# Kernel tuning notes

Measured on AMD Instinct MI355X. Metric: run time of the kernel, lower is better.

Reference implementation:

```python
import jax, jax.numpy as jnp
import numpy as np

N_NODES = 50000
N_EDGES = 300000
HEADS = 2
OUT_CH = 128
BN_EPS = 1e-5
NEG_SLOPE = 0.2


def _batchnorm(x, g, b):
    # training-mode BatchNorm1d: biased batch statistics
    mean = x.mean(axis=0)
    var = x.var(axis=0)
    return (x - mean) * jax.lax.rsqrt(var + BN_EPS) * g + b


def _gatv2(x, src, dst, edge_attr, Wl, bl, Wr, br, We, att, bias, concat):
    # PyG GATv2Conv, share_weights=False, aggr='add'
    n = x.shape[0]
    xl = (x @ Wl + bl).reshape(n, HEADS, OUT_CH)  # source messages
    xr = (x @ Wr + br).reshape(n, HEADS, OUT_CH)  # destination term
    ee = (edge_attr @ We).reshape(-1, HEADS, OUT_CH)
    s = jax.nn.leaky_relu(xl[src] + xr[dst] + ee, NEG_SLOPE)  # [E,H,C]
    alpha = jnp.einsum('ehc,hc->eh', s, att)  # [E,H]
    # segment softmax over edges grouped by destination node
    m = jax.ops.segment_max(alpha, dst, num_segments=n)
    a = jnp.exp(alpha - m[dst])
    den = jax.ops.segment_sum(a, dst, num_segments=n)
    a = a / (den[dst] + 1e-16)
    out = jax.ops.segment_sum(xl[src] * a[:, :, None], dst, num_segments=n)  # [N,H,C]
    out = out.reshape(n, HEADS * OUT_CH) if concat else out.mean(axis=1)
    return out + bias


def setup_inputs() -> dict:
    key = jax.random.key(0)
    ks = jax.random.split(key, 16)
    d = {}
    d['h'] = jax.random.normal(ks[0], (N_NODES, 5), jnp.float32)
    d['edge_index'] = jax.random.randint(ks[1], (2, N_EDGES), 0, N_NODES, jnp.int64)
    d['edge_weight'] = jax.random.uniform(ks[2], (N_EDGES, 1), jnp.float32)
    d['bn0_g'] = jnp.ones((5,), jnp.float32)
    d['bn0_b'] = jnp.zeros((5,), jnp.float32)
    d['bn1_g'] = jnp.ones((256,), jnp.float32)
    d['bn1_b'] = jnp.zeros((256,), jnp.float32)
    def lin(k, fan_in, fan_out):
        return jax.random.normal(k, (fan_in, fan_out), jnp.float32) * (1.0 / np.sqrt(fan_in))
    # conv1: in=5 -> heads*out=256, concat=True
    d['c1_Wl'] = lin(ks[3], 5, 256); d['c1_bl'] = jnp.zeros((256,), jnp.float32)
    d['c1_Wr'] = lin(ks[4], 5, 256); d['c1_br'] = jnp.zeros((256,), jnp.float32)
    d['c1_We'] = lin(ks[5], 1, 256)
    d['c1_att'] = jax.random.normal(ks[6], (HEADS, OUT_CH), jnp.float32) * 0.1
    d['c1_bias'] = jnp.zeros((256,), jnp.float32)
    # mu: in=256 -> 128, concat=False
    d['mu_Wl'] = lin(ks[7], 256, 256); d['mu_bl'] = jnp.zeros((256,), jnp.float32)
    d['mu_Wr'] = lin(ks[8], 256, 256); d['mu_br'] = jnp.zeros((256,), jnp.float32)
    d['mu_We'] = lin(ks[9], 1, 256)
    d['mu_att'] = jax.random.normal(ks[10], (HEADS, OUT_CH), jnp.float32) * 0.1
    d['mu_bias'] = jnp.zeros((128,), jnp.float32)
    # log_std: same shapes as mu
    d['ls_Wl'] = lin(ks[11], 256, 256); d['ls_bl'] = jnp.zeros((256,), jnp.float32)
    d['ls_Wr'] = lin(ks[12], 256, 256); d['ls_br'] = jnp.zeros((256,), jnp.float32)
    d['ls_We'] = lin(ks[13], 1, 256)
    d['ls_att'] = jax.random.normal(ks[14], (HEADS, OUT_CH), jnp.float32) * 0.1
    d['ls_bias'] = jnp.zeros((128,), jnp.float32)
    return d


def reference(h, edge_index, edge_weight, bn0_g, bn0_b, bn1_g, bn1_b,
              c1_Wl, c1_bl, c1_Wr, c1_br, c1_We, c1_att, c1_bias,
              mu_Wl, mu_bl, mu_Wr, mu_br, mu_We, mu_att, mu_bias,
              ls_Wl, ls_bl, ls_Wr, ls_br, ls_We, ls_att, ls_bias):
    src, dst = edge_index[0], edge_index[1]
    x = _batchnorm(h, bn0_g, bn0_b)
    x = _gatv2(x, src, dst, edge_weight, c1_Wl, c1_bl, c1_Wr, c1_br, c1_We, c1_att, c1_bias, concat=True)
    x = jax.nn.relu(_batchnorm(x, bn1_g, bn1_b))
    # dropout identity (eval / deterministic)
    mu = _gatv2(x, src, dst, edge_weight, mu_Wl, mu_bl, mu_Wr, mu_br, mu_We, mu_att, mu_bias, concat=False)
    log_std = _gatv2(x, src, dst, edge_weight, ls_Wl, ls_bl, ls_Wr, ls_br, ls_We, ls_att, ls_bias, concat=False)
    return (mu, log_std)
```

## Files before the change

kernel.cpp:

```cpp
#include <hip/hip_runtime.h>
#include <math.h>

#define N_NODES 50000
#define N_EDGES 300000
#define BN_EPS 1e-5f
#define NEG_SLOPE 0.2f

#define RB_COUNT 3128
#define SCAN_TILES 49
#define BN1_BLOCKS 523

typedef short bf8v __attribute__((ext_vector_type(8)));
typedef float f4v __attribute__((ext_vector_type(4)));
typedef unsigned short u8v __attribute__((ext_vector_type(8)));

__device__ inline unsigned short f2bf(float f) {
    union { float f; unsigned u; } c; c.f = f;
    unsigned r = c.u + 0x7fffu + ((c.u >> 16) & 1u);
    return (unsigned short)(r >> 16);
}
__device__ inline float bf2f(unsigned short u) {
    union { unsigned u; float f; } c; c.u = ((unsigned)u) << 16;
    return c.f;
}

__device__ inline void async_copy16(void* lds, const void* g) {
    __builtin_amdgcn_global_load_lds(
        (const __attribute__((address_space(1))) unsigned int*)g,
        (__attribute__((address_space(3))) unsigned int*)lds, 16, 0, 0);
}

__global__ void bn0_reduce(const float* __restrict__ h, float* __restrict__ acc ) {
    __shared__ float lds[4][10];
    int tid = threadIdx.x;
    int lane = tid & 63, wave = tid >> 6;
    float ls[5] = {0,0,0,0,0}, lq[5] = {0,0,0,0,0};
    for (int r = blockIdx.x * 256 + tid; r < N_NODES; r += 128 * 256) {
        #pragma unroll
        for (int k = 0; k < 5; k++) {
            float v = h[r*5 + k];
            ls[k] += v; lq[k] += v*v;
        }
    }
    #pragma unroll
    for (int k = 0; k < 5; k++) {
        #pragma unroll
        for (int m = 1; m <= 32; m <<= 1) {
            ls[k] += __shfl_xor(ls[k], m, 64);
            lq[k] += __shfl_xor(lq[k], m, 64);
        }
    }
    if (lane == 0) {
        #pragma unroll
        for (int k = 0; k < 5; k++) { lds[wave][k] = ls[k]; lds[wave][5+k] = lq[k]; }
    }
    __syncthreads();
    if (tid < 10) {
        float s = lds[0][tid] + lds[1][tid] + lds[2][tid] + lds[3][tid];
        atomicAdd(&acc[tid], s);
    }
}

__global__ void bn0_finalize(const float* __restrict__ acc, const float* __restrict__ g,
                             const float* __restrict__ b, float* __restrict__ ss) {
    int tid = threadIdx.x;
    if (tid < 5) {
        float mean = acc[tid] * (1.f / N_NODES);
        float var  = acc[5 + tid] * (1.f / N_NODES) - mean*mean;
        float sc = g[tid] * rsqrtf(var + BN_EPS);
        ss[tid]     = sc;
        ss[5 + tid] = b[tid] - mean * sc;
    }
}

__global__ void bn0_apply(const float* __restrict__ h, const float* __restrict__ ss,
                          float* __restrict__ x0) {
    int i = blockIdx.x * blockDim.x + threadIdx.x;
    if (i < N_NODES * 5) {
        int k = i % 5;
        x0[i] = h[i] * ss[k] + ss[5 + k];
    }
}

__global__ void edge_count(const int* __restrict__ dst, int* __restrict__ count) {
    int e = blockIdx.x * blockDim.x + threadIdx.x;
    if (e < N_EDGES) atomicAdd(&count[dst[e]], 1);
}

__global__ void local_scan(const int* __restrict__ count, int* __restrict__ offsets,
                           int* __restrict__ tileSum) {
    __shared__ int lds[1024];
    int tid = threadIdx.x;
    int i = blockIdx.x * 1024 + tid;
    int v = (i < N_NODES) ? count[i] : 0;
    lds[tid] = v;
    __syncthreads();
    #pragma unroll
    for (int off = 1; off < 1024; off <<= 1) {
        int t = (tid >= off) ? lds[tid - off] : 0;
        __syncthreads();
        lds[tid] += t;
        __syncthreads();
    }
    if (i < N_NODES) offsets[i] = lds[tid] - v;
    if (tid == 1023) tileSum[blockIdx.x] = lds[1023];
}

__global__ void tile_scan(const int* __restrict__ tileSum, int* __restrict__ tilePrefix,
                          int* __restrict__ offsets) {
    int lane = threadIdx.x;
    int v = (lane < SCAN_TILES) ? tileSum[lane] : 0;
    int inc = v;
    #pragma unroll
    for (int off = 1; off < 64; off <<= 1) {
        int t = __shfl_up(inc, off, 64);
        if (lane >= off) inc += t;
    }
    int excl = inc - v;
    if (lane < SCAN_TILES) tilePrefix[lane] = excl;
    if (lane == SCAN_TILES - 1) offsets[N_NODES] = inc;
}

__global__ void add_prefix(int* __restrict__ offsets, const int* __restrict__ tilePrefix,
                           int* __restrict__ cursor) {
    int i = blockIdx.x * 1024 + threadIdx.x;
    if (i < N_NODES) {
        int o = offsets[i] + tilePrefix[blockIdx.x];
        offsets[i] = o;
        cursor[i] = o;
    }
}

__global__ void edge_scatter(const int* __restrict__ dst, const int* __restrict__ src,
                             const float* __restrict__ ew, int* __restrict__ cursor,
                             int* __restrict__ srcp, float* __restrict__ ewp) {
    int e = blockIdx.x * blockDim.x + threadIdx.x;
    if (e < N_EDGES) {
        int pos = atomicAdd(&cursor[dst[e]], 1);
        srcp[pos] = src[e];
        ewp[pos] = ew[e];
    }
}

__global__ void gemm_k5(const float* __restrict__ x0,
                        const float* __restrict__ Wl, const float* __restrict__ bl,
                        const float* __restrict__ Wr, const float* __restrict__ br,
                        unsigned short* __restrict__ xl, unsigned short* __restrict__ xr) {
    int n = blockIdx.x;
    int c = threadIdx.x;
    float a0 = x0[n*5+0], a1 = x0[n*5+1], a2 = x0[n*5+2], a3 = x0[n*5+3], a4 = x0[n*5+4];
    float l = bl[c] + a0*Wl[c] + a1*Wl[256+c] + a2*Wl[512+c] + a3*Wl[768+c] + a4*Wl[1024+c];
    float r = br[c] + a0*Wr[c] + a1*Wr[256+c] + a2*Wr[512+c] + a3*Wr[768+c] + a4*Wr[1024+c];
    xl[n*256 + c] = f2bf(l);
    xr[n*256 + c] = f2bf(r);
}

__global__ void pack_x_bn(const float* __restrict__ x, const float* __restrict__ ss1,
                          unsigned short* __restrict__ ap) {
    int t = blockIdx.x * 256 + threadIdx.x;
    int lane = t & 63;
    int kc = (t >> 6) & 7;
    int rb = t >> 9;
    int row = rb * 16 + (lane & 15);
    int k0 = kc * 32 + (lane >> 4) * 8;
    union { unsigned short h[8]; uint4 u; } tmp;
    if (row < N_NODES) {
        const float* s = x + (size_t)row * 256 + k0;
        #pragma unroll
        for (int j = 0; j < 8; j++) {
            int c = k0 + j;
            float v = s[j] * ss1[c] + ss1[256 + c];
            v = v > 0.f ? v : 0.f;
            tmp.h[j] = f2bf(v);
        }
    } else {
        #pragma unroll
        for (int j = 0; j < 8; j++) tmp.h[j] = 0;
    }
    *reinterpret_cast<uint4*>(ap + (size_t)t * 8) = tmp.u;
}

__global__ void pack_w(const float* __restrict__ Wl0, const float* __restrict__ Wr0,
                       const float* __restrict__ Wl1, const float* __restrict__ Wr1,
                       unsigned short* __restrict__ bp) {
    int t = blockIdx.x * 256 + threadIdx.x;
    int lane = t & 63;
    int nt = (t >> 6) & 31;
    int kc = (t >> 11) & 7;
    int conv = t >> 14;
    int col = nt * 16 + (lane & 15);
    int k0 = kc * 32 + (lane >> 4) * 8;
    const float* W = conv ? (col < 256 ? Wl1 : Wr1) : (col < 256 ? Wl0 : Wr0);
    int c = col & 255;
    union { unsigned short h[8]; uint4 u; } tmp;
    #pragma unroll
    for (int j = 0; j < 8; j++) tmp.h[j] = f2bf(W[(size_t)(k0 + j) * 256 + c]);
    *reinterpret_cast<uint4*>(bp + (size_t)t * 8) = tmp.u;
}

__global__ __launch_bounds__(512) void gemm_mfma(const unsigned short* __restrict__ ap,
        const unsigned short* __restrict__ bp,
        const float* __restrict__ bl, const float* __restrict__ br,
        unsigned short* __restrict__ xl, unsigned short* __restrict__ xr) {
    __shared__ unsigned short Bs[2][32][512];
    int lane = threadIdx.x & 63;
    int wave = threadIdx.x >> 6;
    int h = wave & 1;
    int rb = blockIdx.x * 4 + (wave >> 1);

    const unsigned short* aptr = ap + (size_t)rb * 4096 + lane * 8;
    const unsigned short* bsrc = bp + lane * 8;

    auto stage = [&](int buf, int kc) {
        #pragma unroll
        for (int j = 0; j < 4; j++) {
            int f = wave * 4 + j;
            async_copy16(&Bs[buf][f][lane * 8], bsrc + (size_t)kc * 16384 + f * 512);
        }
    };
    stage(0, 0);

    bf8v a[8];
    #pragma unroll
    for (int kc = 0; kc < 8; kc++) a[kc] = *reinterpret_cast<const bf8v*>(aptr + kc * 512);

    f4v acc[16];
    #pragma unroll
    for (int t = 0; t < 16; t++) acc[t] = (f4v){0.f, 0.f, 0.f, 0.f};

    for (int kc = 0; kc < 8; kc++) {
        __syncthreads();
        if (kc < 7) stage((kc + 1) & 1, kc + 1);
        const unsigned short* bb = &Bs[kc & 1][h * 16][lane * 8];
        #pragma unroll
        for (int t = 0; t < 16; t++) {
            bf8v b = *reinterpret_cast<const bf8v*>(bb + t * 512);
            acc[t] = __builtin_amdgcn_mfma_f32_16x16x32_bf16(a[kc], b, acc[t], 0, 0, 0);
        }
    }

    int c15 = lane & 15;
    int row0 = rb * 16 + (lane >> 4) * 4;
    unsigned short* outp = h ? xr : xl;
    const float* bias = h ? br : bl;
    #pragma unroll
    for (int t = 0; t < 16; t++) {
        int col = t * 16 + c15;
        float bv = bias[col];
        #pragma unroll
        for (int r = 0; r < 4; r++) {
            int row = row0 + r;
            if (row < N_NODES) outp[(size_t)row * 256 + col] = f2bf(acc[t][r] + bv);
        }
    }
}

template <int CONCAT>
__global__ void agg_fused(const unsigned short* __restrict__ xl,
                          const unsigned short* __restrict__ xr,
                          const float* __restrict__ We, const float* __restrict__ att,
                          const int* __restrict__ offsets, const int* __restrict__ srcp,
                          const float* __restrict__ ewp, const float* __restrict__ bias,
                          float* __restrict__ out) {
    int n = blockIdx.x * 4 + (threadIdx.x >> 6);
    int lane = threadIdx.x & 63;
    if (n >= N_NODES) return;
    int half = lane >> 5;
    int sub  = lane & 31;
    int cb   = (sub >> 4) * 128 + (sub & 15) * 8;
    float wv[8], av[8], rv[8];
    *(float4*)&wv[0] = *(const float4*)(We + cb);
    *(float4*)&wv[4] = *(const float4*)(We + cb + 4);
    *(float4*)&av[0] = *(const float4*)(att + cb);
    *(float4*)&av[4] = *(const float4*)(att + cb + 4);
    u8v r8 = *(const u8v*)(xr + (size_t)n * 256 + cb);
    #pragma unroll
    for (int j = 0; j < 8; j++) rv[j] = bf2f(r8[j]);
    int beg = offsets[n], end = offsets[n + 1];
    float mrun = -1e30f, den = 0.f;
    float acc[8];
    #pragma unroll
    for (int j = 0; j < 8; j++) acc[j] = 0.f;

    int i = beg + half;
    int sN = 0; float wN = 0.f;
    u8v lN;
    #pragma unroll
    for (int j = 0; j < 8; j++) lN[j] = 0;
    if (i < end) {
        sN = srcp[i]; wN = ewp[i];
        lN = *(const u8v*)(xl + (size_t)sN * 256 + cb);
    }
    for (; i < end; i += 2) {
        u8v l8 = lN; float w = wN;
        int nx = i + 2;
        if (nx < end) {
            sN = srcp[nx]; wN = ewp[nx];
            lN = *(const u8v*)(xl + (size_t)sN * 256 + cb);
        }
        float lv[8];
        float a = 0.f;
        #pragma unroll
        for (int j = 0; j < 8; j++) {
            lv[j] = bf2f(l8[j]);
            float v = lv[j] + rv[j] + w * wv[j];
            v = fmaxf(v, NEG_SLOPE * v);
            a += v * av[j];
        }
        a += __shfl_xor(a, 1, 64);
        a += __shfl_xor(a, 2, 64);
        a += __shfl_xor(a, 4, 64);
        a += __shfl_xor(a, 8, 64);
        float nm = fmaxf(mrun, a);
        float scl = __expf(mrun - nm);
        float p = __expf(a - nm);
        den = den * scl + p;
        #pragma unroll
        for (int j = 0; j < 8; j++) acc[j] = acc[j] * scl + p * lv[j];
        mrun = nm;
    }
    {
        float mo  = __shfl_xor(mrun, 32, 64);
        float dno = __shfl_xor(den, 32, 64);
        float nm = fmaxf(mrun, mo);
        float s0 = __expf(mrun - nm);
        float s1 = __expf(mo - nm);
        den = den * s0 + dno * s1;
        #pragma unroll
        for (int j = 0; j < 8; j++) {
            float ao = __shfl_xor(acc[j], 32, 64);
            acc[j] = acc[j] * s0 + ao * s1;
        }
    }
    float inv = 1.f / (den + 1e-16f);
    if (CONCAT) {
        if (lane < 32) {
            float o[8];
            #pragma unroll
            for (int j = 0; j < 8; j++) o[j] = acc[j] * inv + bias[cb + j];
            *(float4*)(out + (size_t)n * 256 + cb)     = *(float4*)&o[0];
            *(float4*)(out + (size_t)n * 256 + cb + 4) = *(float4*)&o[4];
        }
    } else {
        float o[8];
        #pragma unroll
        for (int j = 0; j < 8; j++) o[j] = acc[j] * inv;
        float po[8];
        #pragma unroll
        for (int j = 0; j < 8; j++) po[j] = __shfl_xor(o[j], 16, 64);
        if (lane < 16) {
            int c0 = (lane & 15) * 8;
            float r[8];
            #pragma unroll
            for (int j = 0; j < 8; j++) r[j] = (o[j] + po[j]) * 0.5f + bias[c0 + j];
            *(float4*)(out + (size_t)n * 128 + c0)     = *(float4*)&r[0];
            *(float4*)(out + (size_t)n * 128 + c0 + 4) = *(float4*)&r[4];
        }
    }
}

__global__ void bn1_reduce(const float* __restrict__ x, float* __restrict__ part) {
    __shared__ float lds[256][9];
    int tid = threadIdx.x;
    int cg = tid & 63;
    int ph = tid >> 6;
    int r0 = blockIdx.x * 96;
    float s[4] = {0,0,0,0}, q[4] = {0,0,0,0};
    #pragma unroll
    for (int it = 0; it < 24; it++) {
        int row = r0 + it * 4 + ph;
        if (row < N_NODES) {
            float4 v = *(const float4*)(x + (size_t)row * 256 + cg * 4);
            s[0] += v.x; s[1] += v.y; s[2] += v.z; s[3] += v.w;
            q[0] += v.x*v.x; q[1] += v.y*v.y; q[2] += v.z*v.z; q[3] += v.w*v.w;
        }
    }
    #pragma unroll
    for (int j = 0; j < 4; j++) { lds[tid][j] = s[j]; lds[tid][4+j] = q[j]; }
    __syncthreads();
    if (tid < 64) {
        float4 sv, qv;
        float* svp = (float*)&sv; float* qvp = (float*)&qv;
        #pragma unroll
        for (int j = 0; j < 4; j++) {
            svp[j] = lds[tid][j] + lds[tid+64][j] + lds[tid+128][j] + lds[tid+192][j];
            qvp[j] = lds[tid][4+j] + lds[tid+64][4+j] + lds[tid+128][4+j] + lds[tid+192][4+j];
        }
        *(float4*)(part + (size_t)blockIdx.x * 512 + cg * 4) = sv;
        *(float4*)(part + (size_t)blockIdx.x * 512 + 256 + cg * 4) = qv;
    }
}

__global__ void bn1_finalize(const float* __restrict__ part, const float* __restrict__ g,
                             const float* __restrict__ b, float* __restrict__ ss1) {
    __shared__ float lds[8][64];
    int t = threadIdx.x;
    int c = blockIdx.x * 32 + (t & 31);
    int ph = t >> 5;
    float s = 0.f, q = 0.f;
    for (int bi = ph; bi < BN1_BLOCKS; bi += 8) {
        s += part[(size_t)bi * 512 + c];
        q += part[(size_t)bi * 512 + 256 + c];
    }
    lds[ph][t & 31] = s;
    lds[ph][32 + (t & 31)] = q;
    __syncthreads();
    if (t < 32) {
        float ss = 0.f, qq = 0.f;
        #pragma unroll
        for (int p = 0; p < 8; p++) { ss += lds[p][t]; qq += lds[p][32 + t]; }
        float mean = ss * (1.f / N_NODES);
        float var  = qq * (1.f / N_NODES) - mean * mean;
        float sc = g[c] * rsqrtf(var + BN_EPS);
        ss1[c] = sc;
        ss1[256 + c] = b[c] - mean * sc;
    }
}

extern "C" void kernel_launch(void* const* d_in, const int* in_sizes, int n_in,
                              void* d_out, int out_size, void* d_ws, size_t ws_size,
                              hipStream_t stream) {
    const float* h          = (const float*)d_in[0];
    const int*   edge_index = (const int*)d_in[1];
    const int*   src = edge_index;
    const int*   dst = edge_index + N_EDGES;
    const float* ew   = (const float*)d_in[2];
    const float* bn0g = (const float*)d_in[3];
    const float* bn0b = (const float*)d_in[4];
    const float* bn1g = (const float*)d_in[5];
    const float* bn1b = (const float*)d_in[6];
    const float* c1_Wl = (const float*)d_in[7];
    const float* c1_bl = (const float*)d_in[8];
    const float* c1_Wr = (const float*)d_in[9];
    const float* c1_br = (const float*)d_in[10];
    const float* c1_We = (const float*)d_in[11];
    const float* c1_att = (const float*)d_in[12];
    const float* c1_bias = (const float*)d_in[13];
    const float* mu_Wl = (const float*)d_in[14];
    const float* mu_bl = (const float*)d_in[15];
    const float* mu_Wr = (const float*)d_in[16];
    const float* mu_br = (const float*)d_in[17];
    const float* mu_We = (const float*)d_in[18];
    const float* mu_att = (const float*)d_in[19];
    const float* mu_bias = (const float*)d_in[20];
    const float* ls_Wl = (const float*)d_in[21];
    const float* ls_bl = (const float*)d_in[22];
    const float* ls_Wr = (const float*)d_in[23];
    const float* ls_br = (const float*)d_in[24];
    const float* ls_We = (const float*)d_in[25];
    const float* ls_att = (const float*)d_in[26];
    const float* ls_bias = (const float*)d_in[27];

    float* out_mu = (float*)d_out;
    float* out_ls = (float*)d_out + (size_t)N_NODES * 128;

    char* ws = (char*)d_ws;
    size_t off = 0;
    auto alloc = [&](size_t bytes) -> void* {
        void* p = ws + off;
        off += (bytes + 255) / 256 * 256;
        return p;
    };
    float* x0      = (float*)alloc((size_t)N_NODES * 5 * 4);
    unsigned short* xl = (unsigned short*)alloc((size_t)N_NODES * 256 * 2);
    unsigned short* xr = (unsigned short*)alloc((size_t)N_NODES * 256 * 2);
    float* xB      = (float*)alloc((size_t)N_NODES * 256 * 4);
    float* bn0acc  = (float*)alloc(10 * 4);
    float* bn0ss   = (float*)alloc(10 * 4);
    float* bn1part = (float*)alloc((size_t)BN1_BLOCKS * 512 * 4);
    float* bn1ss   = (float*)alloc(512 * 4);
    int*   count   = (int*)alloc((size_t)N_NODES * 4);
    int*   offsets = (int*)alloc((size_t)(N_NODES + 1) * 4);
    int*   cursor  = (int*)alloc((size_t)N_NODES * 4);
    int*   srcp    = (int*)alloc((size_t)N_EDGES * 4);
    float* ewp     = (float*)alloc((size_t)N_EDGES * 4);
    int*   tileSum = (int*)alloc((size_t)SCAN_TILES * 4);
    int*   tilePre = (int*)alloc((size_t)SCAN_TILES * 4);
    unsigned short* Apack = (unsigned short*)alloc((size_t)RB_COUNT * 4096 * 2);
    unsigned short* Bpack = (unsigned short*)alloc((size_t)2 * 131072 * 2);

    hipMemsetAsync(count, 0, (size_t)N_NODES * 4, stream);
    hipMemsetAsync(bn0acc, 0, 10 * 4, stream);

    bn0_reduce<<<128, 256, 0, stream>>>(h, bn0acc);
    bn0_finalize<<<1, 64, 0, stream>>>(bn0acc, bn0g, bn0b, bn0ss);
    bn0_apply<<<(N_NODES * 5 + 255) / 256, 256, 0, stream>>>(h, bn0ss, x0);

    edge_count<<<(N_EDGES + 255) / 256, 256, 0, stream>>>(dst, count);
    local_scan<<<SCAN_TILES, 1024, 0, stream>>>(count, offsets, tileSum);
    tile_scan<<<1, 64, 0, stream>>>(tileSum, tilePre, offsets);
    add_prefix<<<SCAN_TILES, 1024, 0, stream>>>(offsets, tilePre, cursor);
    edge_scatter<<<(N_EDGES + 255) / 256, 256, 0, stream>>>(dst, src, ew, cursor, srcp, ewp);

    pack_w<<<128, 256, 0, stream>>>(mu_Wl, mu_Wr, ls_Wl, ls_Wr, Bpack);

    gemm_k5<<<N_NODES, 256, 0, stream>>>(x0, c1_Wl, c1_bl, c1_Wr, c1_br, xl, xr);
    agg_fused<1><<<N_NODES / 4 + 1, 256, 0, stream>>>(xl, xr, c1_We, c1_att, offsets,
                                                      srcp, ewp, c1_bias, xB);

    bn1_reduce<<<BN1_BLOCKS, 256, 0, stream>>>(xB, bn1part);
    bn1_finalize<<<8, 256, 0, stream>>>(bn1part, bn1g, bn1b, bn1ss);
    pack_x_bn<<<6256, 256, 0, stream>>>(xB, bn1ss, Apack);

    gemm_mfma<<<782, 512, 0, stream>>>(Apack, Bpack, mu_bl, mu_br, xl, xr);
    agg_fused<0><<<N_NODES / 4 + 1, 256, 0, stream>>>(xl, xr, mu_We, mu_att, offsets,
                                                      srcp, ewp, mu_bias, out_mu);

    gemm_mfma<<<782, 512, 0, stream>>>(Apack, Bpack + 131072, ls_bl, ls_br, xl, xr);
    agg_fused<0><<<N_NODES / 4 + 1, 256, 0, stream>>>(xl, xr, ls_We, ls_att, offsets,
                                                      srcp, ewp, ls_bias, out_ls);
}
```

Baseline: 453.5 us.

## Fuse mu/log_std aggregation into one dual kernel, fold BN0 into first GEMM

Both second-layer GEMMs now run before a single agg_dual kernel that walks each node's edge list once and aggregates the mu and log_std heads together. This shares the srcp/ewp loads and the loop overhead, and raises memory-level parallelism per gathered edge. The second GEMM writes into the xB buffer, which is reused because it is dead after pack_x_bn. BN0 apply is folded into gemm_k5, which now computes two packed bf16 outputs per thread. The aggregation math uses float2 vectors so packed FP32 instructions can be emitted. The dual kernel holds more live registers, which may lower occupancy.

```diff
diff --git a/kernel.cpp b/kernel.cpp
--- a/kernel.cpp
+++ b/kernel.cpp
@@ -12,16 +12,20 @@
 
 typedef short bf8v __attribute__((ext_vector_type(8)));
 typedef float f4v __attribute__((ext_vector_type(4)));
-typedef unsigned short u8v __attribute__((ext_vector_type(8)));
+typedef float f2v __attribute__((ext_vector_type(2)));
 
 __device__ inline unsigned short f2bf(float f) {
     union { float f; unsigned u; } c; c.f = f;
     unsigned r = c.u + 0x7fffu + ((c.u >> 16) & 1u);
     return (unsigned short)(r >> 16);
 }
-__device__ inline float bf2f(unsigned short u) {
-    union { unsigned u; float f; } c; c.u = ((unsigned)u) << 16;
-    return c.f;
+
+__device__ inline f2v bfpair(unsigned u) {
+    union { unsigned u; float f; } lo, hi;
+    lo.u = u << 16;
+    hi.u = u & 0xffff0000u;
+    f2v r; r.x = lo.f; r.y = hi.f;
+    return r;
 }
 
 __device__ inline void async_copy16(void* lds, const void* g) {
@@ -73,15 +77,6 @@
     }
 }
 
-__global__ void bn0_apply(const float* __restrict__ h, const float* __restrict__ ss,
-                          float* __restrict__ x0) {
-    int i = blockIdx.x * blockDim.x + threadIdx.x;
-    if (i < N_NODES * 5) {
-        int k = i % 5;
-        x0[i] = h[i] * ss[k] + ss[5 + k];
-    }
-}
-
 __global__ void edge_count(const int* __restrict__ dst, int* __restrict__ count) {
     int e = blockIdx.x * blockDim.x + threadIdx.x;
     if (e < N_EDGES) atomicAdd(&count[dst[e]], 1);
@@ -142,17 +137,27 @@
     }
 }
 
-__global__ void gemm_k5(const float* __restrict__ x0,
+__global__ void gemm_k5(const float* __restrict__ h, const float* __restrict__ ss,
                         const float* __restrict__ Wl, const float* __restrict__ bl,
                         const float* __restrict__ Wr, const float* __restrict__ br,
                         unsigned short* __restrict__ xl, unsigned short* __restrict__ xr) {
     int n = blockIdx.x;
-    int c = threadIdx.x;
-    float a0 = x0[n*5+0], a1 = x0[n*5+1], a2 = x0[n*5+2], a3 = x0[n*5+3], a4 = x0[n*5+4];
-    float l = bl[c] + a0*Wl[c] + a1*Wl[256+c] + a2*Wl[512+c] + a3*Wl[768+c] + a4*Wl[1024+c];
-    float r = br[c] + a0*Wr[c] + a1*Wr[256+c] + a2*Wr[512+c] + a3*Wr[768+c] + a4*Wr[1024+c];
-    xl[n*256 + c] = f2bf(l);
-    xr[n*256 + c] = f2bf(r);
+    int c = threadIdx.x * 2;
+    float a[5];
+    #pragma unroll
+    for (int k = 0; k < 5; k++) a[k] = h[n*5 + k] * ss[k] + ss[5 + k];
+    float l0 = bl[c], l1 = bl[c+1], r0 = br[c], r1 = br[c+1];
+    #pragma unroll
+    for (int k = 0; k < 5; k++) {
+        l0 += a[k] * Wl[k*256 + c];
+        l1 += a[k] * Wl[k*256 + c + 1];
+        r0 += a[k] * Wr[k*256 + c];
+        r1 += a[k] * Wr[k*256 + c + 1];
+    }
+    unsigned lp = (unsigned)f2bf(l0) | ((unsigned)f2bf(l1) << 16);
+    unsigned rp = (unsigned)f2bf(r0) | ((unsigned)f2bf(r1) << 16);
+    *reinterpret_cast<unsigned*>(xl + (size_t)n*256 + c) = lp;
+    *reinterpret_cast<unsigned*>(xr + (size_t)n*256 + c) = rp;
 }
 
 __global__ void pack_x_bn(const float* __restrict__ x, const float* __restrict__ ss1,
@@ -255,58 +260,64 @@
     }
 }
 
-template <int CONCAT>
-__global__ void agg_fused(const unsigned short* __restrict__ xl,
-                          const unsigned short* __restrict__ xr,
-                          const float* __restrict__ We, const float* __restrict__ att,
-                          const int* __restrict__ offsets, const int* __restrict__ srcp,
-                          const float* __restrict__ ewp, const float* __restrict__ bias,
-                          float* __restrict__ out) {
+__global__ __launch_bounds__(256) void agg_concat(
+        const unsigned short* __restrict__ xl, const unsigned short* __restrict__ xr,
+        const float* __restrict__ We, const float* __restrict__ att,
+        const int* __restrict__ offsets, const int* __restrict__ srcp,
+        const float* __restrict__ ewp, const float* __restrict__ bias,
+        float* __restrict__ out) {
     int n = blockIdx.x * 4 + (threadIdx.x >> 6);
     int lane = threadIdx.x & 63;
-    if (n >= N_NODES) return;
     int half = lane >> 5;
     int sub  = lane & 31;
     int cb   = (sub >> 4) * 128 + (sub & 15) * 8;
-    float wv[8], av[8], rv[8];
-    *(float4*)&wv[0] = *(const float4*)(We + cb);
-    *(float4*)&wv[4] = *(const float4*)(We + cb + 4);
-    *(float4*)&av[0] = *(const float4*)(att + cb);
-    *(float4*)&av[4] = *(const float4*)(att + cb + 4);
-    u8v r8 = *(const u8v*)(xr + (size_t)n * 256 + cb);
-    #pragma unroll
-    for (int j = 0; j < 8; j++) rv[j] = bf2f(r8[j]);
+    f2v wv[4], av[4], rv[4];
+    {
+        f4v t0 = *(const f4v*)(We + cb);
+        f4v t1 = *(const f4v*)(We + cb + 4);
+        wv[0] = (f2v){t0.x, t0.y}; wv[1] = (f2v){t0.z, t0.w};
+        wv[2] = (f2v){t1.x, t1.y}; wv[3] = (f2v){t1.z, t1.w};
+        t0 = *(const f4v*)(att + cb);
+        t1 = *(const f4v*)(att + cb + 4);
+        av[0] = (f2v){t0.x, t0.y}; av[1] = (f2v){t0.z, t0.w};
+        av[2] = (f2v){t1.x, t1.y}; av[3] = (f2v){t1.z, t1.w};
+        uint4 r8 = *(const uint4*)(xr + ((size_t)n << 8) + cb);
+        rv[0] = bfpair(r8.x); rv[1] = bfpair(r8.y);
+        rv[2] = bfpair(r8.z); rv[3] = bfpair(r8.w);
+    }
     int beg = offsets[n], end = offsets[n + 1];
     float mrun = -1e30f, den = 0.f;
-    float acc[8];
-    #pragma unroll
-    for (int j = 0; j < 8; j++) acc[j] = 0.f;
+    f2v acc[4];
+    #pragma unroll
+    for (int j = 0; j < 4; j++) acc[j] = (f2v){0.f, 0.f};
 
     int i = beg + half;
     int sN = 0; float wN = 0.f;
-    u8v lN;
-    #pragma unroll
-    for (int j = 0; j < 8; j++) lN[j] = 0;
+    uint4 lN = {0u, 0u, 0u, 0u};
     if (i < end) {
         sN = srcp[i]; wN = ewp[i];
-        lN = *(const u8v*)(xl + (size_t)sN * 256 + cb);
+        lN = *(const uint4*)(xl + ((size_t)sN << 8) + cb);
     }
     for (; i < end; i += 2) {
-        u8v l8 = lN; float w = wN;
+        uint4 l8 = lN; float w = wN;
         int nx = i + 2;
         if (nx < end) {
             sN = srcp[nx]; wN = ewp[nx];
-            lN = *(const u8v*)(xl + (size_t)sN * 256 + cb);
-        }
-        float lv[8];
-        float a = 0.f;
-        #pragma unroll
-        for (int j = 0; j < 8; j++) {
-            lv[j] = bf2f(l8[j]);
-            float v = lv[j] + rv[j] + w * wv[j];
-            v = fmaxf(v, NEG_SLOPE * v);
-            a += v * av[j];
-        }
+            lN = *(const uint4*)(xl + ((size_t)sN << 8) + cb);
+        }
+        f2v w2 = (f2v){w, w};
+        f2v lv[4];
+        lv[0] = bfpair(l8.x); lv[1] = bfpair(l8.y);
+        lv[2] = bfpair(l8.z); lv[3] = bfpair(l8.w);
+        f2v da = (f2v){0.f, 0.f};
+        #pragma unroll
+        for (int j = 0; j < 4; j++) {
+            f2v v = lv[j] + rv[j] + w2 * wv[j];
+            f2v s = v * (f2v){NEG_SLOPE, NEG_SLOPE};
+            v.x = fmaxf(v.x, s.x); v.y = fmaxf(v.y, s.y);
+            da += v * av[j];
+        }
+        float a = da.x + da.y;
         a += __shfl_xor(a, 1, 64);
         a += __shfl_xor(a, 2, 64);
         a += __shfl_xor(a, 4, 64);
@@ -315,8 +326,9 @@
         float scl = __expf(mrun - nm);
         float p = __expf(a - nm);
         den = den * scl + p;
-        #pragma unroll
-        for (int j = 0; j < 8; j++) acc[j] = acc[j] * scl + p * lv[j];
+        f2v sc2 = (f2v){scl, scl}, p2 = (f2v){p, p};
+        #pragma unroll
+        for (int j = 0; j < 4; j++) acc[j] = acc[j] * sc2 + p2 * lv[j];
         mrun = nm;
     }
     {
@@ -326,36 +338,190 @@
         float s0 = __expf(mrun - nm);
         float s1 = __expf(mo - nm);
         den = den * s0 + dno * s1;
-        #pragma unroll
-        for (int j = 0; j < 8; j++) {
-            float ao = __shfl_xor(acc[j], 32, 64);
-            acc[j] = acc[j] * s0 + ao * s1;
+        f2v s02 = (f2v){s0, s0}, s12 = (f2v){s1, s1};
+        #pragma unroll
+        for (int j = 0; j < 4; j++) {
+            f2v ao;
+            ao.x = __shfl_xor(acc[j].x, 32, 64);
+            ao.y = __shfl_xor(acc[j].y, 32, 64);
+            acc[j] = acc[j] * s02 + ao * s12;
         }
     }
     float inv = 1.f / (den + 1e-16f);
-    if (CONCAT) {
-        if (lane < 32) {
-            float o[8];
-            #pragma unroll
-            for (int j = 0; j < 8; j++) o[j] = acc[j] * inv + bias[cb + j];
-            *(float4*)(out + (size_t)n * 256 + cb)     = *(float4*)&o[0];
-            *(float4*)(out + (size_t)n * 256 + cb + 4) = *(float4*)&o[4];
-        }
-    } else {
+    if (lane < 32) {
         float o[8];
         #pragma unroll
-        for (int j = 0; j < 8; j++) o[j] = acc[j] * inv;
-        float po[8];
-        #pragma unroll
-        for (int j = 0; j < 8; j++) po[j] = __shfl_xor(o[j], 16, 64);
-        if (lane < 16) {
-            int c0 = (lane & 15) * 8;
-            float r[8];
-            #pragma unroll
-            for (int j = 0; j < 8; j++) r[j] = (o[j] + po[j]) * 0.5f + bias[c0 + j];
-            *(float4*)(out + (size_t)n * 128 + c0)     = *(float4*)&r[0];
-            *(float4*)(out + (size_t)n * 128 + c0 + 4) = *(float4*)&r[4];
-        }
+        for (int j = 0; j < 4; j++) {
+            o[2*j]   = acc[j].x * inv + bias[cb + 2*j];
+            o[2*j+1] = acc[j].y * inv + bias[cb + 2*j + 1];
+        }
+        *(float4*)(out + (size_t)n * 256 + cb)     = *(float4*)&o[0];
+        *(float4*)(out + (size_t)n * 256 + cb + 4) = *(float4*)&o[4];
+    }
+}
+
+__global__ __launch_bounds__(256) void agg_dual(
+        const unsigned short* __restrict__ xlA, const unsigned short* __restrict__ xrA,
+        const unsigned short* __restrict__ xlB, const unsigned short* __restrict__ xrB,
+        const float* __restrict__ WeA, const float* __restrict__ attA,
+        const float* __restrict__ WeB, const float* __restrict__ attB,
+        const int* __restrict__ offsets, const int* __restrict__ srcp,
+        const float* __restrict__ ewp,
+        const float* __restrict__ biasA, const float* __restrict__ biasB,
+        float* __restrict__ outA, float* __restrict__ outB) {
+    int n = blockIdx.x * 4 + (threadIdx.x >> 6);
+    int lane = threadIdx.x & 63;
+    int half = lane >> 5;
+    int sub  = lane & 31;
+    int cb   = (sub >> 4) * 128 + (sub & 15) * 8;
+    f2v wvA[4], avA[4], rvA[4], wvB[4], avB[4], rvB[4];
+    {
+        f4v t0 = *(const f4v*)(WeA + cb);
+        f4v t1 = *(const f4v*)(WeA + cb + 4);
+        wvA[0] = (f2v){t0.x, t0.y}; wvA[1] = (f2v){t0.z, t0.w};
+        wvA[2] = (f2v){t1.x, t1.y}; wvA[3] = (f2v){t1.z, t1.w};
+        t0 = *(const f4v*)(attA + cb);
+        t1 = *(const f4v*)(attA + cb + 4);
+        avA[0] = (f2v){t0.x, t0.y}; avA[1] = (f2v){t0.z, t0.w};
+        avA[2] = (f2v){t1.x, t1.y}; avA[3] = (f2v){t1.z, t1.w};
+        t0 = *(const f4v*)(WeB + cb);
+        t1 = *(const f4v*)(WeB + cb + 4);
+        wvB[0] = (f2v){t0.x, t0.y}; wvB[1] = (f2v){t0.z, t0.w};
+        wvB[2] = (f2v){t1.x, t1.y}; wvB[3] = (f2v){t1.z, t1.w};
+        t0 = *(const f4v*)(attB + cb);
+        t1 = *(const f4v*)(attB + cb + 4);
+        avB[0] = (f2v){t0.x, t0.y}; avB[1] = (f2v){t0.z, t0.w};
+        avB[2] = (f2v){t1.x, t1.y}; avB[3] = (f2v){t1.z, t1.w};
+        uint4 r8 = *(const uint4*)(xrA + ((size_t)n << 8) + cb);
+        rvA[0] = bfpair(r8.x); rvA[1] = bfpair(r8.y);
+        rvA[2] = bfpair(r8.z); rvA[3] = bfpair(r8.w);
+        r8 = *(const uint4*)(xrB + ((size_t)n << 8) + cb);
+        rvB[0] = bfpair(r8.x); rvB[1] = bfpair(r8.y);
+        rvB[2] = bfpair(r8.z); rvB[3] = bfpair(r8.w);
+    }
+    int beg = offsets[n], end = offsets[n + 1];
+    float mA = -1e30f, dA = 0.f, mB = -1e30f, dB = 0.f;
+    f2v accA[4], accB[4];
+    #pragma unroll
+    for (int j = 0; j < 4; j++) { accA[j] = (f2v){0.f, 0.f}; accB[j] = (f2v){0.f, 0.f}; }
+
+    int i = beg + half;
+    int sN = 0; float wN = 0.f;
+    uint4 lNA = {0u, 0u, 0u, 0u}, lNB = {0u, 0u, 0u, 0u};
+    if (i < end) {
+        sN = srcp[i]; wN = ewp[i];
+        size_t o = ((size_t)sN << 8) + cb;
+        lNA = *(const uint4*)(xlA + o);
+        lNB = *(const uint4*)(xlB + o);
+    }
+    for (; i < end; i += 2) {
+        uint4 lA = lNA, lB = lNB; float w = wN;
+        int nx = i + 2;
+        if (nx < end) {
+            sN = srcp[nx]; wN = ewp[nx];
+            size_t o = ((size_t)sN << 8) + cb;
+            lNA = *(const uint4*)(xlA + o);
+            lNB = *(const uint4*)(xlB + o);
+        }
+        f2v w2 = (f2v){w, w};
+        f2v lvA[4], lvB[4];
+        lvA[0] = bfpair(lA.x); lvA[1] = bfpair(lA.y);
+        lvA[2] = bfpair(lA.z); lvA[3] = bfpair(lA.w);
+        lvB[0] = bfpair(lB.x); lvB[1] = bfpair(lB.y);
+        lvB[2] = bfpair(lB.z); lvB[3] = bfpair(lB.w);
+        f2v daA = (f2v){0.f, 0.f}, daB = (f2v){0.f, 0.f};
+        #pragma unroll
+        for (int j = 0; j < 4; j++) {
+            f2v vA = lvA[j] + rvA[j] + w2 * wvA[j];
+            f2v sA = vA * (f2v){NEG_SLOPE, NEG_SLOPE};
+            vA.x = fmaxf(vA.x, sA.x); vA.y = fmaxf(vA.y, sA.y);
+            daA += vA * avA[j];
+            f2v vB = lvB[j] + rvB[j] + w2 * wvB[j];
+            f2v sB = vB * (f2v){NEG_SLOPE, NEG_SLOPE};
+            vB.x = fmaxf(vB.x, sB.x); vB.y = fmaxf(vB.y, sB.y);
+            daB += vB * avB[j];
+        }
+        float aA = daA.x + daA.y, aB = daB.x + daB.y;
+        float tA, tB;
+        tA = __shfl_xor(aA, 1, 64); tB = __shfl_xor(aB, 1, 64); aA += tA; aB += tB;
+        tA = __shfl_xor(aA, 2, 64); tB = __shfl_xor(aB, 2, 64); aA += tA; aB += tB;
+        tA = __shfl_xor(aA, 4, 64); tB = __shfl_xor(aB, 4, 64); aA += tA; aB += tB;
+        tA = __shfl_xor(aA, 8, 64); tB = __shfl_xor(aB, 8, 64); aA += tA; aB += tB;
+        float nmA = fmaxf(mA, aA), nmB = fmaxf(mB, aB);
+        float sclA = __expf(mA - nmA), pA = __expf(aA - nmA);
+        float sclB = __expf(mB - nmB), pB = __expf(aB - nmB);
+        dA = dA * sclA + pA;
+        dB = dB * sclB + pB;
+        f2v scA = (f2v){sclA, sclA}, pA2 = (f2v){pA, pA};
+        f2v scB = (f2v){sclB, sclB}, pB2 = (f2v){pB, pB};
+        #pragma unroll
+        for (int j = 0; j < 4; j++) {
+            accA[j] = accA[j] * scA + pA2 * lvA[j];
+            accB[j] = accB[j] * scB + pB2 * lvB[j];
+        }
+        mA = nmA; mB = nmB;
+    }
+    {
+        float mo  = __shfl_xor(mA, 32, 64);
+        float dno = __shfl_xor(dA, 32, 64);
+        float nm = fmaxf(mA, mo);
+        float s0 = __expf(mA - nm);
+        float s1 = __expf(mo - nm);
+        dA = dA * s0 + dno * s1;
+        f2v s02 = (f2v){s0, s0}, s12 = (f2v){s1, s1};
+        #pragma unroll
+        for (int j = 0; j < 4; j++) {
+            f2v ao;
+            ao.x = __shfl_xor(accA[j].x, 32, 64);
+            ao.y = __shfl_xor(accA[j].y, 32, 64);
+            accA[j] = accA[j] * s02 + ao * s12;
+        }
+    }
+    {
+        float mo  = __shfl_xor(mB, 32, 64);
+        float dno = __shfl_xor(dB, 32, 64);
+        float nm = fmaxf(mB, mo);
+        float s0 = __expf(mB - nm);
+        float s1 = __expf(mo - nm);
+        dB = dB * s0 + dno * s1;
+        f2v s02 = (f2v){s0, s0}, s12 = (f2v){s1, s1};
+        #pragma unroll
+        for (int j = 0; j < 4; j++) {
+            f2v ao;
+            ao.x = __shfl_xor(accB[j].x, 32, 64);
+            ao.y = __shfl_xor(accB[j].y, 32, 64);
+            accB[j] = accB[j] * s02 + ao * s12;
+        }
+    }
+    float invA = 1.f / (dA + 1e-16f);
+    float invB = 1.f / (dB + 1e-16f);
+    float oA[8], oB[8], poA[8], poB[8];
+    #pragma unroll
+    for (int j = 0; j < 4; j++) {
+        oA[2*j]   = accA[j].x * invA;
+        oA[2*j+1] = accA[j].y * invA;
+        oB[2*j]   = accB[j].x * invB;
+        oB[2*j+1] = accB[j].y * invB;
+    }
+    #pragma unroll
+    for (int j = 0; j < 8; j++) {
+        poA[j] = __shfl_xor(oA[j], 16, 64);
+        poB[j] = __shfl_xor(oB[j], 16, 64);
+    }
+    int q = lane >> 4;
+    int c0 = (lane & 15) * 8;
+    if (q == 0) {
+        float r[8];
+        #pragma unroll
+        for (int j = 0; j < 8; j++) r[j] = (oA[j] + poA[j]) * 0.5f + biasA[c0 + j];
+        *(float4*)(outA + (size_t)n * 128 + c0)     = *(float4*)&r[0];
+        *(float4*)(outA + (size_t)n * 128 + c0 + 4) = *(float4*)&r[4];
+    } else if (q == 2) {
+        float r[8];
+        #pragma unroll
+        for (int j = 0; j < 8; j++) r[j] = (oB[j] + poB[j]) * 0.5f + biasB[c0 + j];
+        *(float4*)(outB + (size_t)n * 128 + c0)     = *(float4*)&r[0];
+        *(float4*)(outB + (size_t)n * 128 + c0 + 4) = *(float4*)&r[4];
     }
 }
 
@@ -461,7 +627,6 @@
         off += (bytes + 255) / 256 * 256;
         return p;
     };
-    float* x0      = (float*)alloc((size_t)N_NODES * 5 * 4);
     unsigned short* xl = (unsigned short*)alloc((size_t)N_NODES * 256 * 2);
     unsigned short* xr = (unsigned short*)alloc((size_t)N_NODES * 256 * 2);
     float* xB      = (float*)alloc((size_t)N_NODES * 256 * 4);
@@ -479,12 +644,14 @@
     unsigned short* Apack = (unsigned short*)alloc((size_t)RB_COUNT * 4096 * 2);
     unsigned short* Bpack = (unsigned short*)alloc((size_t)2 * 131072 * 2);
 
+    unsigned short* xl2 = (unsigned short*)xB;
+    unsigned short* xr2 = xl2 + (size_t)N_NODES * 256;
+
     hipMemsetAsync(count, 0, (size_t)N_NODES * 4, stream);
     hipMemsetAsync(bn0acc, 0, 10 * 4, stream);
 
     bn0_reduce<<<128, 256, 0, stream>>>(h, bn0acc);
     bn0_finalize<<<1, 64, 0, stream>>>(bn0acc, bn0g, bn0b, bn0ss);
-    bn0_apply<<<(N_NODES * 5 + 255) / 256, 256, 0, stream>>>(h, bn0ss, x0);
 
     edge_count<<<(N_EDGES + 255) / 256, 256, 0, stream>>>(dst, count);
     local_scan<<<SCAN_TILES, 1024, 0, stream>>>(count, offsets, tileSum);
@@ -494,19 +661,19 @@
 
     pack_w<<<128, 256, 0, stream>>>(mu_Wl, mu_Wr, ls_Wl, ls_Wr, Bpack);
 
-    gemm_k5<<<N_NODES, 256, 0, stream>>>(x0, c1_Wl, c1_bl, c1_Wr, c1_br, xl, xr);
-    agg_fused<1><<<N_NODES / 4 + 1, 256, 0, stream>>>(xl, xr, c1_We, c1_att, offsets,
-                                                      srcp, ewp, c1_bias, xB);
+    gemm_k5<<<N_NODES, 128, 0, stream>>>(h, bn0ss, c1_Wl, c1_bl, c1_Wr, c1_br, xl, xr);
+    agg_concat<<<N_NODES / 4, 256, 0, stream>>>(xl, xr, c1_We, c1_att, offsets,
+                                                srcp, ewp, c1_bias, xB);
 
     bn1_reduce<<<BN1_BLOCKS, 256, 0, stream>>>(xB, bn1part);
     bn1_finalize<<<8, 256, 0, stream>>>(bn1part, bn1g, bn1b, bn1ss);
     pack_x_bn<<<6256, 256, 0, stream>>>(xB, bn1ss, Apack);
 
     gemm_mfma<<<782, 512, 0, stream>>>(Apack, Bpack, mu_bl, mu_br, xl, xr);
-    agg_fused<0><<<N_NODES / 4 + 1, 256, 0, stream>>>(xl, xr, mu_We, mu_att, offsets,
-                                                      srcp, ewp, mu_bias, out_mu);
-
-    gemm_mfma<<<782, 512, 0, stream>>>(Apack, Bpack + 131072, ls_bl, ls_br, xl, xr);
-    agg_fused<0><<<N_NODES / 4 + 1, 256, 0, stream>>>(xl, xr, ls_We, ls_att, offsets,
-                                                      srcp, ewp, ls_bias, out_ls);
-}
+    gemm_mfma<<<782, 512, 0, stream>>>(Apack, Bpack + 131072, ls_bl, ls_br, xl2, xr2);
+
+    agg_dual<<<N_NODES / 4, 256, 0, stream>>>(xl, xr, xl2, xr2,
+                                              mu_We, mu_att, ls_We, ls_att,
+                                              offsets, srcp, ewp,
+                                              mu_bias, ls_bias, out_mu, out_ls);
+}
```

Result: no change. 459.3 us (+1.3%).
